# Kernel optimization log

Hardware: AMD Instinct MI355X
Metric: run time of the kernel (lower is better)

Reference implementation:

```python
import jax, jax.numpy as jnp
import numpy as np

N, E, G = 50000, 600000, 128
ND, ED, H, T, L = 32, 16, 128, 128, 4


def setup_inputs() -> dict:
    key = jax.random.key(0)
    ks = jax.random.split(key, 32)
    s = 0.05
    nrm = lambda k, shp: (jax.random.normal(k, shp, jnp.float32) * s)
    inp = {
        'node_f': jax.random.normal(ks[0], (N, ND), jnp.float32),
        'node_x': jax.random.normal(ks[1], (N, 3), jnp.float32),
        'edge_w': jax.random.normal(ks[2], (E, ED), jnp.float32),
        'src': jax.random.randint(ks[3], (E,), 0, N, jnp.int32),
        'dst': jax.random.randint(ks[4], (E,), 0, N, jnp.int32),
        'graph_ids': jnp.sort(jax.random.randint(ks[5], (N,), 0, G, jnp.int32)),
        'W_in': nrm(ks[6], (ND, H)), 'b_in': jnp.zeros((H,), jnp.float32),
        'W_e': nrm(ks[7], (ED, H)), 'b_e': jnp.zeros((H,), jnp.float32),
        'msg_W1': nrm(ks[8], (L, 3 * H + 1, H)), 'msg_b1': jnp.zeros((L, H), jnp.float32),
        'msg_W2': nrm(ks[9], (L, H, H)), 'msg_b2': jnp.zeros((L, H), jnp.float32),
        'upd_W1': nrm(ks[10], (L, H, H)), 'upd_b1': jnp.zeros((L, H), jnp.float32),
        'upd_W2': nrm(ks[11], (L, H, H)), 'upd_b2': jnp.zeros((L, H), jnp.float32),
        'W_out': nrm(ks[12], (2 * H, T)), 'b_out': jnp.zeros((T,), jnp.float32),
    }
    return inp


def reference(node_f, node_x, edge_w, src, dst, graph_ids,
              W_in, b_in, W_e, b_e,
              msg_W1, msg_b1, msg_W2, msg_b2,
              upd_W1, upd_b1, upd_W2, upd_b2,
              W_out, b_out):
    relu = jax.nn.relu
    # input node / edge embeddings
    f = relu(node_f @ W_in + b_in)            # [N, H]
    w = relu(edge_w @ W_e + b_e)              # [E, H]
    # squared distance per edge (positions are static across layers)
    sq = jnp.sum((node_x[src] - node_x[dst]) ** 2, axis=-1, keepdims=True)  # [E, 1]
    for i in range(L):
        mi = jnp.concatenate([f[src], f[dst], w, sq], axis=-1)  # [E, 3H+1]
        m = relu(relu(mi @ msg_W1[i] + msg_b1[i]) @ msg_W2[i] + msg_b2[i])  # [E, H]
        m_sum = jax.ops.segment_sum(m, dst, num_segments=N)     # scatter-sum to dst
        u = m_sum + f
        f = relu(relu(u @ upd_W1[i] + upd_b1[i]) @ upd_W2[i] + upd_b2[i])
    # per-graph mean / max readout
    counts = jax.ops.segment_sum(jnp.ones((N,), f.dtype), graph_ids, num_segments=G)
    mean = jax.ops.segment_sum(f, graph_ids, num_segments=G) / jnp.maximum(counts, 1.0)[:, None]
    mx = jax.ops.segment_max(f, graph_ids, num_segments=G)
    mx = jnp.where(counts[:, None] > 0, mx, 0.0)
    return jnp.concatenate([mean, mx], axis=-1) @ W_out + b_out  # [G, T]
```

## Files before the change

kernel.cpp:

```cpp
#include <hip/hip_runtime.h>
#include <hip/hip_fp16.h>

typedef _Float16 f16;
typedef _Float16 f16x8 __attribute__((ext_vector_type(8)));
typedef float f32x4 __attribute__((ext_vector_type(4)));

#define N_NODES 50000
#define N_EDGES 600000
#define G_GRAPHS 128
#define H 128
#define NP 50176
#define NT_E 18750
#define NB_E 1024
#define NT_N 1563

__global__ void k_f0(const float* __restrict__ node_f, const float* __restrict__ W_in,
                     const float* __restrict__ b_in, f16* __restrict__ fh)
{
    __shared__ float sW[32 * 128];
    __shared__ float sx[8][32];
    const int tid = threadIdx.x;
    const int base = blockIdx.x * 8;
    for (int i = tid; i < 32 * 128; i += 128) sW[i] = W_in[i];
    for (int i = tid; i < 8 * 32; i += 128) {
        int u = i >> 5, k = i & 31;
        int n = base + u;
        sx[u][k] = (n < N_NODES) ? node_f[(size_t)n * 32 + k] : 0.0f;
    }
    __syncthreads();
    const float bj = b_in[tid];
    #pragma unroll
    for (int u = 0; u < 8; ++u) {
        int n = base + u;
        if (n >= N_NODES) break;
        float acc = bj;
        #pragma unroll
        for (int k = 0; k < 32; ++k) acc = fmaf(sx[u][k], sW[k * 128 + tid], acc);
        fh[(size_t)n * H + tid] = (f16)fmaxf(acc, 0.0f);
    }
}

__global__ void k_hist(const int* __restrict__ dst, int* __restrict__ cnt)
{
    int e = blockIdx.x * 256 + threadIdx.x;
    if (e < N_EDGES) atomicAdd(&cnt[dst[e]], 1);
}

__global__ void k_scanA(const int* __restrict__ cnt, int* __restrict__ rowptr,
                        int* __restrict__ bsum)
{
    __shared__ int s[256];
    const int t = threadIdx.x;
    const int i = blockIdx.x * 256 + t;
    int v = cnt[i];
    s[t] = v;
    __syncthreads();
    #pragma unroll
    for (int off = 1; off < 256; off <<= 1) {
        int x = (t >= off) ? s[t - off] : 0;
        __syncthreads();
        s[t] += x;
        __syncthreads();
    }
    rowptr[i] = s[t] - v;
    if (t == 255) bsum[blockIdx.x] = s[255];
}

__global__ void k_scanB(const int* __restrict__ bsum, int* __restrict__ boff)
{
    __shared__ int s[256];
    const int t = threadIdx.x;
    int v = (t < 196) ? bsum[t] : 0;
    s[t] = v;
    __syncthreads();
    #pragma unroll
    for (int off = 1; off < 256; off <<= 1) {
        int x = (t >= off) ? s[t - off] : 0;
        __syncthreads();
        s[t] += x;
        __syncthreads();
    }
    boff[t] = s[t] - v;
}

__global__ void k_scanC(int* __restrict__ rowptr, const int* __restrict__ boff)
{
    int i = blockIdx.x * 256 + threadIdx.x;
    rowptr[i] += boff[blockIdx.x];
}

__global__ void k_scatter_idx(const int* __restrict__ dst, const int* __restrict__ rowptr,
                              int* __restrict__ fill, int* __restrict__ perm_eidx)
{
    int e = blockIdx.x * 256 + threadIdx.x;
    if (e >= N_EDGES) return;
    int d = dst[e];
    int p = rowptr[d] + atomicAdd(&fill[d], 1);
    perm_eidx[p] = e;
}

__global__ void k_gather(const int* __restrict__ perm_eidx, const float* __restrict__ edge_w,
                         const int* __restrict__ src, const int* __restrict__ dst,
                         const float* __restrict__ node_x,
                         int* __restrict__ perm_src, int* __restrict__ perm_dst,
                         float* __restrict__ perm_sq, f16* __restrict__ perm_ewh)
{
    int pp = blockIdx.x * 256 + threadIdx.x;
    if (pp >= N_EDGES) return;
    int e = perm_eidx[pp];
    int s = src[e], d = dst[e];
    float dx = node_x[s * 3 + 0] - node_x[d * 3 + 0];
    float dy = node_x[s * 3 + 1] - node_x[d * 3 + 1];
    float dz = node_x[s * 3 + 2] - node_x[d * 3 + 2];
    perm_src[pp] = s;
    perm_dst[pp] = d;
    perm_sq[pp] = dx * dx + dy * dy + dz * dz;
    const float4* pw = (const float4*)(edge_w + (size_t)e * 16);
    float4 w0 = pw[0], w1 = pw[1], w2 = pw[2], w3 = pw[3];
    f16x8 v0, v1;
    v0[0] = (f16)w0.x; v0[1] = (f16)w0.y; v0[2] = (f16)w0.z; v0[3] = (f16)w0.w;
    v0[4] = (f16)w1.x; v0[5] = (f16)w1.y; v0[6] = (f16)w1.z; v0[7] = (f16)w1.w;
    v1[0] = (f16)w2.x; v1[1] = (f16)w2.y; v1[2] = (f16)w2.z; v1[3] = (f16)w2.w;
    v1[4] = (f16)w3.x; v1[5] = (f16)w3.y; v1[6] = (f16)w3.z; v1[7] = (f16)w3.w;
    f16x8* q = (f16x8*)(perm_ewh + (size_t)pp * 16);
    q[0] = v0; q[1] = v1;
}

__global__ __launch_bounds__(512, 2) void k_edge2(
    const f16* __restrict__ fh,
    const int* __restrict__ perm_src, const int* __restrict__ perm_dst,
    const float* __restrict__ perm_sq, const f16* __restrict__ perm_ewh,
    const float* __restrict__ W_e, const float* __restrict__ b_e,
    const float* __restrict__ W1, const float* __restrict__ b1,
    const float* __restrict__ W2, const float* __restrict__ b2,
    f16* __restrict__ msum)
{
    const int tid = threadIdx.x;
    const int wave = tid >> 6;
    const int lane = tid & 63;
    const int l16 = lane & 15;
    const int lq  = lane >> 4;
    const int col = wave * 16 + l16;

    f16x8 wef, w1f[12], w2f[4];
    #pragma unroll
    for (int j = 0; j < 8; ++j) {
        int k = lq * 8 + j;
        wef[j] = (k < 16) ? (f16)W_e[(size_t)k * H + col] : (f16)0.0f;
    }
    #pragma unroll
    for (int k = 0; k < 12; ++k)
        #pragma unroll
        for (int j = 0; j < 8; ++j)
            w1f[k][j] = (f16)W1[(size_t)(k * 32 + lq * 8 + j) * H + col];
    #pragma unroll
    for (int k = 0; k < 4; ++k)
        #pragma unroll
        for (int j = 0; j < 8; ++j)
            w2f[k][j] = (f16)W2[(size_t)(k * 32 + lq * 8 + j) * H + col];
    const float w1last = W1[(size_t)384 * H + col];
    const float b1v = b1[col], b2v = b2[col], bev = b_e[col];

    __shared__ alignas(16) f16 Atile[32][392];
    __shared__ alignas(16) f16 h1B[2][32][136];
    __shared__ int   s_src[2][32];
    __shared__ int   s_dst[2][32];
    __shared__ float s_sq[2][32];

    const int b = ((blockIdx.x & 7) << 7) | (blockIdx.x >> 3);
    const int t0 = (int)((long)b * NT_E / NB_E);
    const int t1 = (int)((long)(b + 1) * NT_E / NB_E);

    const int srow = tid >> 4, sch = tid & 15;
    const int sj = ((srow >> 2) & 3) * 8 + ((srow >> 4) << 2) + (srow & 3);

    if (tid < 32) {
        int e = t0 * 32 + tid;
        s_src[0][tid] = perm_src[e];
        s_dst[0][tid] = perm_dst[e];
        s_sq[0][tid]  = perm_sq[e];
    }
    __syncthreads();
    int4 rs_, rd_;
    {
        int sv = s_src[0][sj], dv = s_dst[0][sj];
        rs_ = ((const int4*)(fh + (size_t)sv * H))[sch];
        rd_ = ((const int4*)(fh + (size_t)dv * H))[sch];
    }
    f16x8 rew[2];
    #pragma unroll
    for (int m = 0; m < 2; ++m) {
        if (lq < 2) {
            int j = (l16 >> 2) * 8 + m * 4 + (l16 & 3);
            rew[m] = *(const f16x8*)(perm_ewh + (size_t)(t0 * 32 + j) * 16 + lq * 8);
        }
    }
    int mr_s = 0, mr_d = 0; float mr_q = 0.0f;
    if (tid < 32) {
        int e = min((t0 + 1) * 32 + tid, N_EDGES - 1);
        mr_s = perm_src[e]; mr_d = perm_dst[e]; mr_q = perm_sq[e];
    }
    ((int4*)&Atile[srow][0])[sch]   = rs_;
    ((int4*)&Atile[srow][128])[sch] = rd_;

    int P = 0, Q = 0;
    for (int t = t0; t < t1; ++t, P ^= 1, Q ^= 1) {
        #pragma unroll
        for (int m = 0; m < 2; ++m) {
            f16x8 a;
            if (lq < 2) {
                a = rew[m];
            } else {
                #pragma unroll
                for (int jj = 0; jj < 8; ++jj) a[jj] = (f16)0.0f;
            }
            f32x4 c = {bev, bev, bev, bev};
            c = __builtin_amdgcn_mfma_f32_16x16x32_f16(a, wef, c, 0, 0, 0);
            #pragma unroll
            for (int r = 0; r < 4; ++r)
                Atile[m * 16 + lq * 4 + r][256 + col] = (f16)fmaxf(c[r], 0.0f);
        }
        if (tid < 32) {
            s_src[P ^ 1][tid] = mr_s;
            s_dst[P ^ 1][tid] = mr_d;
            s_sq[P ^ 1][tid]  = mr_q;
        }
        __syncthreads();

        int dc[8];
        f32x4 acc1[2];
        #pragma unroll
        for (int m = 0; m < 2; ++m)
            #pragma unroll
            for (int r = 0; r < 4; ++r) {
                int j = lq * 8 + m * 4 + r;
                dc[m * 4 + r] = s_dst[P][j];
                acc1[m][r] = fmaf(s_sq[P][j], w1last, b1v);
            }
        if (t + 1 < t1) {
            int sv = s_src[P ^ 1][sj], dv = s_dst[P ^ 1][sj];
            rs_ = ((const int4*)(fh + (size_t)sv * H))[sch];
            rd_ = ((const int4*)(fh + (size_t)dv * H))[sch];
            #pragma unroll
            for (int m = 0; m < 2; ++m) {
                if (lq < 2) {
                    int j = (l16 >> 2) * 8 + m * 4 + (l16 & 3);
                    rew[m] = *(const f16x8*)(perm_ewh + (size_t)((t + 1) * 32 + j) * 16 + lq * 8);
                }
            }
        }
        if (tid < 32) {
            int e = min((t + 2) * 32 + tid, N_EDGES - 1);
            mr_s = perm_src[e]; mr_d = perm_dst[e]; mr_q = perm_sq[e];
        }
        #pragma unroll
        for (int k = 0; k < 12; ++k) {
            #pragma unroll
            for (int m = 0; m < 2; ++m) {
                f16x8 a = *(const f16x8*)&Atile[m * 16 + l16][k * 32 + lq * 8];
                acc1[m] = __builtin_amdgcn_mfma_f32_16x16x32_f16(a, w1f[k], acc1[m], 0, 0, 0);
            }
        }
        #pragma unroll
        for (int m = 0; m < 2; ++m)
            #pragma unroll
            for (int r = 0; r < 4; ++r)
                h1B[Q][m * 16 + lq * 4 + r][col] = (f16)fmaxf(acc1[m][r], 0.0f);
        __syncthreads();

        f32x4 acc2[2];
        #pragma unroll
        for (int m = 0; m < 2; ++m) {
            f32x4 c = {b2v, b2v, b2v, b2v};
            acc2[m] = c;
        }
        #pragma unroll
        for (int k = 0; k < 4; ++k) {
            #pragma unroll
            for (int m = 0; m < 2; ++m) {
                f16x8 a = *(const f16x8*)&h1B[Q][m * 16 + l16][k * 32 + lq * 8];
                acc2[m] = __builtin_amdgcn_mfma_f32_16x16x32_f16(a, w2f[k], acc2[m], 0, 0, 0);
            }
        }
        {
            float run = fmaxf(acc2[0][0], 0.0f);
            int cd = dc[0];
            #pragma unroll
            for (int i = 1; i < 8; ++i) {
                float v = fmaxf(acc2[i >> 2][i & 3], 0.0f);
                int d = dc[i];
                if (d == cd) {
                    run += v;
                } else {
                    float nb = __shfl_xor(run, 1);
                    if ((l16 & 1) == 0) {
                        union { f16 h[2]; __half2 v2; } u;
                        u.h[0] = (f16)run; u.h[1] = (f16)nb;
                        unsafeAtomicAdd((__half2*)&msum[(size_t)cd * H + col], u.v2);
                    }
                    run = v; cd = d;
                }
            }
            float nb = __shfl_xor(run, 1);
            if ((l16 & 1) == 0) {
                union { f16 h[2]; __half2 v2; } u;
                u.h[0] = (f16)run; u.h[1] = (f16)nb;
                unsafeAtomicAdd((__half2*)&msum[(size_t)cd * H + col], u.v2);
            }
        }
        if (t + 1 < t1) {
            ((int4*)&Atile[srow][0])[sch]   = rs_;
            ((int4*)&Atile[srow][128])[sch] = rd_;
        }
    }
}

__global__ __launch_bounds__(256, 3) void k_update(
    const f16* __restrict__ msum, f16* __restrict__ fh,
    const float* __restrict__ W1, const float* __restrict__ b1,
    const float* __restrict__ W2, const float* __restrict__ b2)
{
    const int tid = threadIdx.x;
    const int wave = tid >> 6;
    const int lane = tid & 63;
    const int l16 = lane & 15;
    const int lq = lane >> 4;
    const int colbase = wave * 32;

    f16x8 w1fr[4][2], w2fr[4][2];
    float b1v[2], b2v[2];
    #pragma unroll
    for (int nt = 0; nt < 2; ++nt) {
        const int col = colbase + nt * 16 + l16;
        #pragma unroll
        for (int k = 0; k < 4; ++k) {
            f16x8 v1, v2;
            #pragma unroll
            for (int j = 0; j < 8; ++j) {
                v1[j] = (f16)W1[(size_t)(k * 32 + lq * 8 + j) * H + col];
                v2[j] = (f16)W2[(size_t)(k * 32 + lq * 8 + j) * H + col];
            }
            w1fr[k][nt] = v1;
            w2fr[k][nt] = v2;
        }
        b1v[nt] = b1[col];
        b2v[nt] = b2[col];
    }

    __shared__ alignas(16) f16 U[32][136];
    __shared__ alignas(16) f16 h1b[32][136];
    const int row = tid >> 3, ch = tid & 7;

    int tile = blockIdx.x;
    f16x8 rm0, rm1, rf0, rf1;
    if (tile < NT_N) {
        int n = min(tile * 32 + row, N_NODES - 1);
        const f16x8* pm = (const f16x8*)(msum + (size_t)n * H) + ch * 2;
        const f16x8* pf = (const f16x8*)(fh + (size_t)n * H) + ch * 2;
        rm0 = pm[0]; rm1 = pm[1]; rf0 = pf[0]; rf1 = pf[1];
    }
    for (; tile < NT_N; tile += gridDim.x) {
        const int n0 = tile * 32;
        {
            f16 tmp[16];
            #pragma unroll
            for (int j = 0; j < 8; ++j) {
                tmp[j]     = (f16)((float)rm0[j] + (float)rf0[j]);
                tmp[8 + j] = (f16)((float)rm1[j] + (float)rf1[j]);
            }
            int4* q0 = (int4*)(&U[row][ch * 16]);
            q0[0] = ((const int4*)tmp)[0];
            q0[1] = ((const int4*)tmp)[1];
        }
        {
            int nt_ = tile + gridDim.x;
            if (nt_ < NT_N) {
                int n = min(nt_ * 32 + row, N_NODES - 1);
                const f16x8* pm = (const f16x8*)(msum + (size_t)n * H) + ch * 2;
                const f16x8* pf = (const f16x8*)(fh + (size_t)n * H) + ch * 2;
                rm0 = pm[0]; rm1 = pm[1]; rf0 = pf[0]; rf1 = pf[1];
            }
        }
        __syncthreads();

        f32x4 acc[2][2];
        #pragma unroll
        for (int m = 0; m < 2; ++m)
            #pragma unroll
            for (int nt = 0; nt < 2; ++nt) {
                f32x4 c = {b1v[nt], b1v[nt], b1v[nt], b1v[nt]};
                acc[m][nt] = c;
            }
        #pragma unroll
        for (int k = 0; k < 4; ++k) {
            #pragma unroll
            for (int m = 0; m < 2; ++m) {
                f16x8 a = *(const f16x8*)&U[m * 16 + l16][k * 32 + lq * 8];
                #pragma unroll
                for (int nt = 0; nt < 2; ++nt)
                    acc[m][nt] = __builtin_amdgcn_mfma_f32_16x16x32_f16(a, w1fr[k][nt], acc[m][nt], 0, 0, 0);
            }
        }
        #pragma unroll
        for (int m = 0; m < 2; ++m)
            #pragma unroll
            for (int nt = 0; nt < 2; ++nt)
                #pragma unroll
                for (int r = 0; r < 4; ++r)
                    h1b[m * 16 + lq * 4 + r][colbase + nt * 16 + l16] = (f16)fmaxf(acc[m][nt][r], 0.0f);
        __syncthreads();

        f32x4 acc2[2][2];
        #pragma unroll
        for (int m = 0; m < 2; ++m)
            #pragma unroll
            for (int nt = 0; nt < 2; ++nt) {
                f32x4 c = {b2v[nt], b2v[nt], b2v[nt], b2v[nt]};
                acc2[m][nt] = c;
            }
        #pragma unroll
        for (int k = 0; k < 4; ++k) {
            #pragma unroll
            for (int m = 0; m < 2; ++m) {
                f16x8 a = *(const f16x8*)&h1b[m * 16 + l16][k * 32 + lq * 8];
                #pragma unroll
                for (int nt = 0; nt < 2; ++nt)
                    acc2[m][nt] = __builtin_amdgcn_mfma_f32_16x16x32_f16(a, w2fr[k][nt], acc2[m][nt], 0, 0, 0);
            }
        }
        #pragma unroll
        for (int m = 0; m < 2; ++m)
            #pragma unroll
            for (int nt = 0; nt < 2; ++nt)
                #pragma unroll
                for (int r = 0; r < 4; ++r) {
                    int rr = m * 16 + lq * 4 + r;
                    int n = n0 + rr;
                    if (n < N_NODES)
                        fh[(size_t)n * H + colbase + nt * 16 + l16] = (f16)fmaxf(acc2[m][nt][r], 0.0f);
                }
    }
}

__global__ void k_readout(const f16* __restrict__ fh, const int* __restrict__ gid,
                          float* __restrict__ gsum, float* __restrict__ gmax,
                          int* __restrict__ gcnt)
{
    __shared__ int s_gid[64];
    const int tid = threadIdx.x;
    const int base = blockIdx.x * 64;
    if (tid < 64) s_gid[tid] = (base + tid < N_NODES) ? gid[base + tid] : -1;
    __syncthreads();
    if (tid < 64 && base + tid < N_NODES) atomicAdd(&gcnt[s_gid[tid]], 1);

    float lsum = 0.0f, lmax = 0.0f;
    int cur = s_gid[0];
    if (cur >= 0) {
        for (int i = 0; i < 64; ++i) {
            int g = s_gid[i];
            if (g < 0) break;
            if (g != cur) {
                unsafeAtomicAdd(&gsum[(size_t)cur * H + tid], lsum);
                atomicMax((int*)&gmax[(size_t)cur * H + tid], __float_as_int(lmax));
                lsum = 0.0f; lmax = 0.0f; cur = g;
            }
            float v = (float)fh[(size_t)(base + i) * H + tid];
            lsum += v;
            lmax = fmaxf(lmax, v);
        }
        unsafeAtomicAdd(&gsum[(size_t)cur * H + tid], lsum);
        atomicMax((int*)&gmax[(size_t)cur * H + tid], __float_as_int(lmax));
    }
}

__global__ void k_out(const float* __restrict__ gsum, const float* __restrict__ gmax,
                      const int* __restrict__ gcnt, const float* __restrict__ W_out,
                      const float* __restrict__ b_out, float* __restrict__ out)
{
    __shared__ float sm[128], sx[128];
    const int g = blockIdx.x, t = threadIdx.x;
    const float inv = 1.0f / fmaxf((float)gcnt[g], 1.0f);
    sm[t] = gsum[(size_t)g * H + t] * inv;
    sx[t] = gmax[(size_t)g * H + t];
    __syncthreads();
    float acc = b_out[t];
    for (int k = 0; k < H; ++k) {
        acc = fmaf(sm[k], W_out[(size_t)k * 128 + t], acc);
        acc = fmaf(sx[k], W_out[(size_t)(128 + k) * 128 + t], acc);
    }
    out[(size_t)g * 128 + t] = acc;
}

extern "C" void kernel_launch(void* const* d_in, const int* in_sizes, int n_in,
                              void* d_out, int out_size, void* d_ws, size_t ws_size,
                              hipStream_t stream)
{
    const float* node_f = (const float*)d_in[0];
    const float* node_x = (const float*)d_in[1];
    const float* edge_w = (const float*)d_in[2];
    const int*   src    = (const int*)d_in[3];
    const int*   dst    = (const int*)d_in[4];
    const int*   gid    = (const int*)d_in[5];
    const float* W_in   = (const float*)d_in[6];
    const float* b_in   = (const float*)d_in[7];
    const float* W_e    = (const float*)d_in[8];
    const float* b_e    = (const float*)d_in[9];
    const float* msg_W1 = (const float*)d_in[10];
    const float* msg_b1 = (const float*)d_in[11];
    const float* msg_W2 = (const float*)d_in[12];
    const float* msg_b2 = (const float*)d_in[13];
    const float* upd_W1 = (const float*)d_in[14];
    const float* upd_b1 = (const float*)d_in[15];
    const float* upd_W2 = (const float*)d_in[16];
    const float* upd_b2 = (const float*)d_in[17];
    const float* W_out  = (const float*)d_in[18];
    const float* b_out  = (const float*)d_in[19];
    float* out = (float*)d_out;

    char* ws = (char*)d_ws;
    size_t off = 0;
    f16*   fh       = (f16*)(ws + off);   off += (size_t)N_NODES * H * 2;
    f16*   perm_ewh = (f16*)(ws + off);   off += (size_t)N_EDGES * 16 * 2;
    int*   perm_src = (int*)(ws + off);   off += (size_t)N_EDGES * 4;
    int*   perm_dst = (int*)(ws + off);   off += (size_t)N_EDGES * 4;
    float* perm_sq  = (float*)(ws + off); off += (size_t)N_EDGES * 4;
    int*   rowptr   = (int*)(ws + off);   off += (size_t)NP * 4;
    int*   cnt      = (int*)(ws + off);   off += (size_t)NP * 4;
    int*   bsum     = (int*)(ws + off);   off += 256 * 4;
    int*   boff     = (int*)(ws + off);   off += 256 * 4;
    f16*   msum     = (f16*)(ws + off);   off += (size_t)N_NODES * H * 2;
    float* gsum     = (float*)(ws + off); off += (size_t)G_GRAPHS * H * 4;
    float* gmax     = (float*)(ws + off); off += (size_t)G_GRAPHS * H * 4;
    int*   gcnt     = (int*)(ws + off);   off += (size_t)G_GRAPHS * 4;
    int*   perm_eidx = (int*)msum;

    k_f0<<<(N_NODES + 7) / 8, 128, 0, stream>>>(node_f, W_in, b_in, fh);

    (void)hipMemsetAsync(cnt, 0, (size_t)NP * 4, stream);
    k_hist<<<(N_EDGES + 255) / 256, 256, 0, stream>>>(dst, cnt);
    k_scanA<<<NP / 256, 256, 0, stream>>>(cnt, rowptr, bsum);
    k_scanB<<<1, 256, 0, stream>>>(bsum, boff);
    k_scanC<<<NP / 256, 256, 0, stream>>>(rowptr, boff);
    (void)hipMemsetAsync(cnt, 0, (size_t)NP * 4, stream);
    k_scatter_idx<<<(N_EDGES + 255) / 256, 256, 0, stream>>>(dst, rowptr, cnt, perm_eidx);
    k_gather<<<(N_EDGES + 255) / 256, 256, 0, stream>>>(perm_eidx, edge_w, src, dst, node_x,
                                                        perm_src, perm_dst, perm_sq, perm_ewh);

    for (int l = 0; l < 4; ++l) {
        (void)hipMemsetAsync(msum, 0, (size_t)N_NODES * H * 2, stream);
        k_edge2<<<NB_E, 512, 0, stream>>>(fh, perm_src, perm_dst, perm_sq, perm_ewh,
                                          W_e, b_e,
                                          msg_W1 + (size_t)l * 385 * H, msg_b1 + (size_t)l * H,
                                          msg_W2 + (size_t)l * H * H,  msg_b2 + (size_t)l * H,
                                          msum);
        k_update<<<512, 256, 0, stream>>>(msum, fh,
                                          upd_W1 + (size_t)l * H * H, upd_b1 + (size_t)l * H,
                                          upd_W2 + (size_t)l * H * H, upd_b2 + (size_t)l * H);
    }

    (void)hipMemsetAsync(gsum, 0, (size_t)G_GRAPHS * H * 4, stream);
    (void)hipMemsetAsync(gmax, 0, (size_t)G_GRAPHS * H * 4, stream);
    (void)hipMemsetAsync(gcnt, 0, (size_t)G_GRAPHS * 4, stream);
    k_readout<<<(N_NODES + 63) / 64, 128, 0, stream>>>(fh, gid, gsum, gmax, gcnt);
    k_out<<<G_GRAPHS, 128, 0, stream>>>(gsum, gmax, gcnt, W_out, b_out, out);
}
```

Before: 1.288 ms.

## Software-pipeline edge message kernel across tiles with one barrier per iteration

Restructures the edge message loop so that the second MLP layer and scatter-add for tile t-1 run in the same iteration as the first layer for tile t. The input tile and index buffers are double- or triple-buffered, which removes the mid-iteration barrier and leaves one __syncthreads per tile. The edge-embedding MFMA for the next tile moves to the end of the iteration, and the last tile is drained in an epilogue. This costs more LDS (the Atile buffer doubles), which may lower occupancy, and the control flow becomes more complex.

```diff
diff --git a/kernel.cpp b/kernel.cpp
--- a/kernel.cpp
+++ b/kernel.cpp
@@ -161,11 +161,11 @@
     const float w1last = W1[(size_t)384 * H + col];
     const float b1v = b1[col], b2v = b2[col], bev = b_e[col];
 
-    __shared__ alignas(16) f16 Atile[32][392];
+    __shared__ alignas(16) f16 Atile[2][32][392];
     __shared__ alignas(16) f16 h1B[2][32][136];
-    __shared__ int   s_src[2][32];
-    __shared__ int   s_dst[2][32];
-    __shared__ float s_sq[2][32];
+    __shared__ int   s_src[3][32];
+    __shared__ int   s_dst[3][32];
+    __shared__ float s_sq[3][32];
 
     const int b = ((blockIdx.x & 7) << 7) | (blockIdx.x >> 3);
     const int t0 = (int)((long)b * NT_E / NB_E);
@@ -175,57 +175,48 @@
     const int sj = ((srow >> 2) & 3) * 8 + ((srow >> 4) << 2) + (srow & 3);
 
     if (tid < 32) {
-        int e = t0 * 32 + tid;
-        s_src[0][tid] = perm_src[e];
-        s_dst[0][tid] = perm_dst[e];
-        s_sq[0][tid]  = perm_sq[e];
+        int e0 = t0 * 32 + tid;
+        s_src[t0 % 3][tid] = perm_src[e0];
+        s_dst[t0 % 3][tid] = perm_dst[e0];
+        s_sq [t0 % 3][tid] = perm_sq[e0];
+        int e1 = min((t0 + 1) * 32 + tid, N_EDGES - 1);
+        s_src[(t0 + 1) % 3][tid] = perm_src[e1];
+        s_dst[(t0 + 1) % 3][tid] = perm_dst[e1];
+        s_sq [(t0 + 1) % 3][tid] = perm_sq[e1];
     }
     __syncthreads();
-    int4 rs_, rd_;
     {
-        int sv = s_src[0][sj], dv = s_dst[0][sj];
-        rs_ = ((const int4*)(fh + (size_t)sv * H))[sch];
-        rd_ = ((const int4*)(fh + (size_t)dv * H))[sch];
-    }
-    f16x8 rew[2];
-    #pragma unroll
-    for (int m = 0; m < 2; ++m) {
-        if (lq < 2) {
-            int j = (l16 >> 2) * 8 + m * 4 + (l16 & 3);
-            rew[m] = *(const f16x8*)(perm_ewh + (size_t)(t0 * 32 + j) * 16 + lq * 8);
-        }
-    }
-    int mr_s = 0, mr_d = 0; float mr_q = 0.0f;
-    if (tid < 32) {
-        int e = min((t0 + 1) * 32 + tid, N_EDGES - 1);
-        mr_s = perm_src[e]; mr_d = perm_dst[e]; mr_q = perm_sq[e];
-    }
-    ((int4*)&Atile[srow][0])[sch]   = rs_;
-    ((int4*)&Atile[srow][128])[sch] = rd_;
-
-    int P = 0, Q = 0;
-    for (int t = t0; t < t1; ++t, P ^= 1, Q ^= 1) {
+        const int pa = t0 & 1;
+        int sv = s_src[t0 % 3][sj], dv = s_dst[t0 % 3][sj];
+        int4 ra = ((const int4*)(fh + (size_t)sv * H))[sch];
+        int4 rb = ((const int4*)(fh + (size_t)dv * H))[sch];
+        ((int4*)&Atile[pa][srow][0])[sch]   = ra;
+        ((int4*)&Atile[pa][srow][128])[sch] = rb;
         #pragma unroll
         for (int m = 0; m < 2; ++m) {
-            f16x8 a;
+            f16x8 aa;
             if (lq < 2) {
-                a = rew[m];
+                int j = (l16 >> 2) * 8 + m * 4 + (l16 & 3);
+                aa = *(const f16x8*)(perm_ewh + (size_t)(t0 * 32 + j) * 16 + lq * 8);
             } else {
                 #pragma unroll
-                for (int jj = 0; jj < 8; ++jj) a[jj] = (f16)0.0f;
+                for (int jj = 0; jj < 8; ++jj) aa[jj] = (f16)0.0f;
             }
             f32x4 c = {bev, bev, bev, bev};
-            c = __builtin_amdgcn_mfma_f32_16x16x32_f16(a, wef, c, 0, 0, 0);
+            c = __builtin_amdgcn_mfma_f32_16x16x32_f16(aa, wef, c, 0, 0, 0);
             #pragma unroll
             for (int r = 0; r < 4; ++r)
-                Atile[m * 16 + lq * 4 + r][256 + col] = (f16)fmaxf(c[r], 0.0f);
-        }
-        if (tid < 32) {
-            s_src[P ^ 1][tid] = mr_s;
-            s_dst[P ^ 1][tid] = mr_d;
-            s_sq[P ^ 1][tid]  = mr_q;
-        }
-        __syncthreads();
+                Atile[pa][m * 16 + lq * 4 + r][256 + col] = (f16)fmaxf(c[r], 0.0f);
+        }
+    }
+    __syncthreads();
+
+    int dcp[8];
+    for (int t = t0; t < t1; ++t) {
+        const int pa = t & 1;
+        const int m0 = t % 3;
+        const int m1 = (t + 1) % 3;
+        const int m2 = (t + 2) % 3;
 
         int dc[8];
         f32x4 acc1[2];
@@ -234,61 +225,52 @@
             #pragma unroll
             for (int r = 0; r < 4; ++r) {
                 int j = lq * 8 + m * 4 + r;
-                dc[m * 4 + r] = s_dst[P][j];
-                acc1[m][r] = fmaf(s_sq[P][j], w1last, b1v);
-            }
-        if (t + 1 < t1) {
-            int sv = s_src[P ^ 1][sj], dv = s_dst[P ^ 1][sj];
+                dc[m * 4 + r] = s_dst[m0][j];
+                acc1[m][r] = fmaf(s_sq[m0][j], w1last, b1v);
+            }
+
+        int4 rs_, rd_;
+        f16x8 rew[2];
+        {
+            int sv = s_src[m1][sj], dv = s_dst[m1][sj];
             rs_ = ((const int4*)(fh + (size_t)sv * H))[sch];
             rd_ = ((const int4*)(fh + (size_t)dv * H))[sch];
             #pragma unroll
             for (int m = 0; m < 2; ++m) {
                 if (lq < 2) {
                     int j = (l16 >> 2) * 8 + m * 4 + (l16 & 3);
-                    rew[m] = *(const f16x8*)(perm_ewh + (size_t)((t + 1) * 32 + j) * 16 + lq * 8);
+                    int e = min((t + 1) * 32 + j, N_EDGES - 1);
+                    rew[m] = *(const f16x8*)(perm_ewh + (size_t)e * 16 + lq * 8);
                 }
             }
         }
+        int mrs = 0, mrd = 0; float mrq = 0.0f;
         if (tid < 32) {
             int e = min((t + 2) * 32 + tid, N_EDGES - 1);
-            mr_s = perm_src[e]; mr_d = perm_dst[e]; mr_q = perm_sq[e];
-        }
-        #pragma unroll
-        for (int k = 0; k < 12; ++k) {
+            mrs = perm_src[e]; mrd = perm_dst[e]; mrq = perm_sq[e];
+        }
+
+        if (t > t0) {
+            f32x4 acc2[2];
             #pragma unroll
             for (int m = 0; m < 2; ++m) {
-                f16x8 a = *(const f16x8*)&Atile[m * 16 + l16][k * 32 + lq * 8];
-                acc1[m] = __builtin_amdgcn_mfma_f32_16x16x32_f16(a, w1f[k], acc1[m], 0, 0, 0);
-            }
-        }
-        #pragma unroll
-        for (int m = 0; m < 2; ++m)
-            #pragma unroll
-            for (int r = 0; r < 4; ++r)
-                h1B[Q][m * 16 + lq * 4 + r][col] = (f16)fmaxf(acc1[m][r], 0.0f);
-        __syncthreads();
-
-        f32x4 acc2[2];
-        #pragma unroll
-        for (int m = 0; m < 2; ++m) {
-            f32x4 c = {b2v, b2v, b2v, b2v};
-            acc2[m] = c;
-        }
-        #pragma unroll
-        for (int k = 0; k < 4; ++k) {
-            #pragma unroll
-            for (int m = 0; m < 2; ++m) {
-                f16x8 a = *(const f16x8*)&h1B[Q][m * 16 + l16][k * 32 + lq * 8];
-                acc2[m] = __builtin_amdgcn_mfma_f32_16x16x32_f16(a, w2f[k], acc2[m], 0, 0, 0);
-            }
-        }
-        {
+                f32x4 c = {b2v, b2v, b2v, b2v};
+                acc2[m] = c;
+            }
+            #pragma unroll
+            for (int k = 0; k < 4; ++k) {
+                #pragma unroll
+                for (int m = 0; m < 2; ++m) {
+                    f16x8 a = *(const f16x8*)&h1B[pa ^ 1][m * 16 + l16][k * 32 + lq * 8];
+                    acc2[m] = __builtin_amdgcn_mfma_f32_16x16x32_f16(a, w2f[k], acc2[m], 0, 0, 0);
+                }
+            }
             float run = fmaxf(acc2[0][0], 0.0f);
-            int cd = dc[0];
+            int cd = dcp[0];
             #pragma unroll
             for (int i = 1; i < 8; ++i) {
                 float v = fmaxf(acc2[i >> 2][i & 3], 0.0f);
-                int d = dc[i];
+                int d = dcp[i];
                 if (d == cd) {
                     run += v;
                 } else {
@@ -308,9 +290,85 @@
                 unsafeAtomicAdd((__half2*)&msum[(size_t)cd * H + col], u.v2);
             }
         }
-        if (t + 1 < t1) {
-            ((int4*)&Atile[srow][0])[sch]   = rs_;
-            ((int4*)&Atile[srow][128])[sch] = rd_;
+
+        #pragma unroll
+        for (int k = 0; k < 12; ++k) {
+            #pragma unroll
+            for (int m = 0; m < 2; ++m) {
+                f16x8 a = *(const f16x8*)&Atile[pa][m * 16 + l16][k * 32 + lq * 8];
+                acc1[m] = __builtin_amdgcn_mfma_f32_16x16x32_f16(a, w1f[k], acc1[m], 0, 0, 0);
+            }
+        }
+        #pragma unroll
+        for (int m = 0; m < 2; ++m)
+            #pragma unroll
+            for (int r = 0; r < 4; ++r)
+                h1B[pa][m * 16 + lq * 4 + r][col] = (f16)fmaxf(acc1[m][r], 0.0f);
+
+        #pragma unroll
+        for (int m = 0; m < 2; ++m) {
+            f16x8 aa;
+            if (lq < 2) {
+                aa = rew[m];
+            } else {
+                #pragma unroll
+                for (int jj = 0; jj < 8; ++jj) aa[jj] = (f16)0.0f;
+            }
+            f32x4 c = {bev, bev, bev, bev};
+            c = __builtin_amdgcn_mfma_f32_16x16x32_f16(aa, wef, c, 0, 0, 0);
+            #pragma unroll
+            for (int r = 0; r < 4; ++r)
+                Atile[pa ^ 1][m * 16 + lq * 4 + r][256 + col] = (f16)fmaxf(c[r], 0.0f);
+        }
+        ((int4*)&Atile[pa ^ 1][srow][0])[sch]   = rs_;
+        ((int4*)&Atile[pa ^ 1][srow][128])[sch] = rd_;
+        if (tid < 32) {
+            s_src[m2][tid] = mrs; s_dst[m2][tid] = mrd; s_sq[m2][tid] = mrq;
+        }
+        #pragma unroll
+        for (int i = 0; i < 8; ++i) dcp[i] = dc[i];
+        __syncthreads();
+    }
+
+    {
+        const int ph = (t1 - 1) & 1;
+        f32x4 acc2[2];
+        #pragma unroll
+        for (int m = 0; m < 2; ++m) {
+            f32x4 c = {b2v, b2v, b2v, b2v};
+            acc2[m] = c;
+        }
+        #pragma unroll
+        for (int k = 0; k < 4; ++k) {
+            #pragma unroll
+            for (int m = 0; m < 2; ++m) {
+                f16x8 a = *(const f16x8*)&h1B[ph][m * 16 + l16][k * 32 + lq * 8];
+                acc2[m] = __builtin_amdgcn_mfma_f32_16x16x32_f16(a, w2f[k], acc2[m], 0, 0, 0);
+            }
+        }
+        float run = fmaxf(acc2[0][0], 0.0f);
+        int cd = dcp[0];
+        #pragma unroll
+        for (int i = 1; i < 8; ++i) {
+            float v = fmaxf(acc2[i >> 2][i & 3], 0.0f);
+            int d = dcp[i];
+            if (d == cd) {
+                run += v;
+            } else {
+                float nb = __shfl_xor(run, 1);
+                if ((l16 & 1) == 0) {
+                    union { f16 h[2]; __half2 v2; } u;
+                    u.h[0] = (f16)run; u.h[1] = (f16)nb;
+                    unsafeAtomicAdd((__half2*)&msum[(size_t)cd * H + col], u.v2);
+                }
+                run = v; cd = d;
+            }
+        }
+        float nb = __shfl_xor(run, 1);
+        if ((l16 & 1) == 0) {
+            union { f16 h[2]; __half2 v2; } u;
+            u.h[0] = (f16)run; u.h[1] = (f16)nb;
+            unsafeAtomicAdd((__half2*)&msum[(size_t)cd * H + col], u.v2);
         }
     }
 }
```

Result: faster. 1.182 ms (-8.2%).
